# Kernel optimization log

Hardware: AMD Instinct MI355X
Metric: run time of the kernel (lower is better)

Reference implementation:

```python
import jax, jax.numpy as jnp
import numpy as np

HIDDEN = 768
FFN = 3072
E = 8
TOP_K = 2


def setup_inputs() -> dict:
    key = jax.random.key(0)
    k_x, k_r, k_w1, k_w2 = jax.random.split(key, 4)
    x = jax.random.normal(k_x, (1, 1024, HIDDEN), dtype=jnp.float32)
    # nn.Linear(hidden, E, bias=False): weight applied as x @ W^T; store as [H, E]
    bound = 1.0 / np.sqrt(HIDDEN)
    router_w = jax.random.uniform(k_r, (HIDDEN, E), minval=-bound, maxval=bound, dtype=jnp.float32)
    w1 = jax.random.normal(k_w1, (E, HIDDEN, FFN), dtype=jnp.float32) * 0.02
    w2 = jax.random.normal(k_w2, (E, FFN, HIDDEN), dtype=jnp.float32) * 0.02
    return {"x": x, "router_w": router_w, "w1": w1, "w2": w2}


def reference(x, router_w, w1, w2):
    B, T, H = x.shape
    xf = x.reshape(-1, H)                                  # [N, H]
    logits = xf @ router_w                                 # [N, E] (eval mode: no noise)
    probs = jax.nn.softmax(logits, axis=-1)
    top_v, top_i = jax.lax.top_k(probs, TOP_K)             # [N, K]
    top_v = top_v / jnp.sum(top_v, axis=-1, keepdims=True)  # renormalize top-k probs
    # Combine top-k weights into a dense per-expert gate; zero gates make the
    # dense per-expert computation mathematically identical to sparse dispatch.
    gates = jnp.sum(jax.nn.one_hot(top_i, E, dtype=xf.dtype) * top_v[..., None], axis=1)  # [N, E]
    h = jax.nn.gelu(jnp.einsum('nh,ehf->enf', xf, w1), approximate=False)  # [E, N, F]
    y = jnp.einsum('enf,efh->enh', h, w2)                  # [E, N, H]
    out = jnp.einsum('ne,enh->nh', gates, y)               # [N, H]
    return out.reshape(B, T, H)
```

## Files before the change

kernel.cpp:

```cpp
#include <hip/hip_runtime.h>
#include <cmath>

#define NTOK 1024
#define HD   768
#define FF   3072
#define NE   8
#define NSLOT (NTOK * 2)

typedef unsigned short u16;
typedef unsigned int   u32;
typedef __bf16 bf16x8 __attribute__((ext_vector_type(8)));
typedef float  f32x4  __attribute__((ext_vector_type(4)));

__device__ __forceinline__ u16 f2bf(float f) {
  union { float f; u32 u; } v; v.f = f;
  u32 r = v.u + 0x7FFFu + ((v.u >> 16) & 1u);
  return (u16)(r >> 16);
}

__global__ __launch_bounds__(256) void router_logits(
    const float* __restrict__ x, const float* __restrict__ rw,
    u16* __restrict__ xb, int* __restrict__ counts,
    int* __restrict__ ti, int* __restrict__ tpos, float* __restrict__ tg)
{
  __shared__ float rwt[NE * HD];
  const int tid = threadIdx.x;
  for (int i = tid; i < NE * HD; i += 256) {
    const int h = i >> 3, e = i & 7;
    rwt[e * HD + h] = rw[i];
  }
  __syncthreads();

  const int wid  = tid >> 6;
  const int lane = tid & 63;
  const int t    = blockIdx.x * 4 + wid;
  const float* xrow = x + (size_t)t * HD;
  u16* xbrow = xb + (size_t)t * HD;

  float acc[NE] = {};
#pragma unroll
  for (int j = 0; j < 12; ++j) {
    const int h = lane + j * 64;
    const float xv = xrow[h];
    xbrow[h] = f2bf(xv);
#pragma unroll
    for (int e = 0; e < NE; ++e) acc[e] += xv * rwt[e * HD + h];
  }
#pragma unroll
  for (int e = 0; e < NE; ++e) {
    float v = acc[e];
#pragma unroll
    for (int off = 32; off; off >>= 1) v += __shfl_down(v, off, 64);
    acc[e] = v;
  }

  if (lane == 0) {
    float v0 = -1e30f, v1 = -1e30f; int i0 = 0, i1 = 0;
#pragma unroll
    for (int e = 0; e < NE; ++e) {
      const float p = acc[e];
      if (p > v0) { v1 = v0; i1 = i0; v0 = p; i0 = e; }
      else if (p > v1) { v1 = p; i1 = e; }
    }
    const float e1 = expf(v1 - v0);
    const float g0 = 1.0f / (1.0f + e1);
    const float g1 = e1 / (1.0f + e1);
    const int p0 = atomicAdd(&counts[i0], 1);
    const int p1 = atomicAdd(&counts[i1], 1);
    ti[2 * t] = i0;  ti[2 * t + 1] = i1;
    tpos[2 * t] = p0; tpos[2 * t + 1] = p1;
    tg[2 * t] = g0;  tg[2 * t + 1] = g1;
  }
}

__global__ __launch_bounds__(1024) void router_scatter(
    const int* __restrict__ counts, const int* __restrict__ ti,
    const int* __restrict__ tpos, const float* __restrict__ tg,
    int* __restrict__ tos, float* __restrict__ gos, int* __restrict__ seg)
{
  __shared__ int offs[NE];
  const int t = threadIdx.x;
  if (t == 0) {
    int o = 0;
    for (int e = 0; e < NE; ++e) {
      offs[e] = o; seg[e] = o; seg[NE + e] = counts[e]; o += counts[e];
    }
  }
  __syncthreads();
  const int i0 = ti[2 * t], i1 = ti[2 * t + 1];
  const int s0 = offs[i0] + tpos[2 * t];
  const int s1 = offs[i1] + tpos[2 * t + 1];
  tos[s0] = t; gos[s0] = tg[2 * t];
  tos[s1] = t; gos[s1] = tg[2 * t + 1];
}

#define LDA 40

__global__ __launch_bounds__(256) void ffn1_kernel(
    const u16* __restrict__ xb, const float* __restrict__ w1,
    const int* __restrict__ tos, const int* __restrict__ seg,
    u16* __restrict__ hbuf)
{
  const int e   = blockIdx.z;
  const int cnt = seg[NE + e];
  const int m0  = blockIdx.y * 64;
  if (m0 >= cnt) return;
  const int start = seg[e];
  const int n0    = blockIdx.x * 64;

  __shared__ __align__(16) u16 As[64 * LDA];
  __shared__ __align__(16) u16 Bs[64 * LDA];
  __shared__ int toks[64];

  const int tid = threadIdx.x;
  if (tid < 64) toks[tid] = tos[start + min(m0 + tid, cnt - 1)];
  __syncthreads();

  const int lane = tid & 63;
  const int wid  = tid >> 6;
  const int wm   = (wid >> 1) << 5;
  const int wn   = (wid & 1) << 5;
  const int q    = lane >> 4;
  const int r16  = lane & 15;

  const int am = tid >> 2;
  const int ak = (tid & 3) << 3;
  const u16* arow = xb + (size_t)toks[am] * HD + ak;
  const int bkw = wid << 3;

  f32x4 acc[2][2] = {};

  for (int k0 = 0; k0 < HD; k0 += 32) {
    {
      const uint4 av = *(const uint4*)(arow + k0);
      *(uint4*)(&As[am * LDA + ak]) = av;
    }
    {
      const float* src = w1 + (size_t)(e * HD + k0 + bkw) * FF + n0 + lane;
      u16 tmp[8];
#pragma unroll
      for (int j = 0; j < 8; ++j) tmp[j] = f2bf(src[(size_t)j * FF]);
      uint4 bv;
      bv.x = (u32)tmp[0] | ((u32)tmp[1] << 16);
      bv.y = (u32)tmp[2] | ((u32)tmp[3] << 16);
      bv.z = (u32)tmp[4] | ((u32)tmp[5] << 16);
      bv.w = (u32)tmp[6] | ((u32)tmp[7] << 16);
      *(uint4*)(&Bs[lane * LDA + bkw]) = bv;
    }
    __syncthreads();
    bf16x8 af0 = *(const bf16x8*)(&As[(wm + r16)      * LDA + (q << 3)]);
    bf16x8 af1 = *(const bf16x8*)(&As[(wm + 16 + r16) * LDA + (q << 3)]);
    bf16x8 bf0 = *(const bf16x8*)(&Bs[(wn + r16)      * LDA + (q << 3)]);
    bf16x8 bf1 = *(const bf16x8*)(&Bs[(wn + 16 + r16) * LDA + (q << 3)]);
    acc[0][0] = __builtin_amdgcn_mfma_f32_16x16x32_bf16(af0, bf0, acc[0][0], 0, 0, 0);
    acc[0][1] = __builtin_amdgcn_mfma_f32_16x16x32_bf16(af0, bf1, acc[0][1], 0, 0, 0);
    acc[1][0] = __builtin_amdgcn_mfma_f32_16x16x32_bf16(af1, bf0, acc[1][0], 0, 0, 0);
    acc[1][1] = __builtin_amdgcn_mfma_f32_16x16x32_bf16(af1, bf1, acc[1][1], 0, 0, 0);
    __syncthreads();
  }

#pragma unroll
  for (int r = 0; r < 2; ++r) {
#pragma unroll
    for (int i = 0; i < 4; ++i) {
      const int mloc = wm + r * 16 + q * 4 + i;
      if (m0 + mloc < cnt) {
        u16* drow = hbuf + (size_t)(start + m0 + mloc) * FF + n0;
#pragma unroll
        for (int c = 0; c < 2; ++c) {
          float v = acc[r][c][i];
          v = 0.5f * v * (1.0f + erff(v * 0.70710678118f));
          drow[wn + c * 16 + r16] = f2bf(v);
        }
      }
    }
  }
}

__global__ __launch_bounds__(256) void ffn2_kernel(
    const u16* __restrict__ hbuf, const float* __restrict__ w2,
    const int* __restrict__ tos, const float* __restrict__ gos,
    const int* __restrict__ seg, float* __restrict__ out)
{
  const int e   = blockIdx.z;
  const int cnt = seg[NE + e];
  const int m0  = blockIdx.y * 64;
  if (m0 >= cnt) return;
  const int start = seg[e];
  const int n0    = blockIdx.x * 64;

  __shared__ __align__(16) u16 As[64 * LDA];
  __shared__ __align__(16) u16 Bs[64 * LDA];
  __shared__ int   toks[64];
  __shared__ float gates[64];

  const int tid = threadIdx.x;
  if (tid < 64) {
    const int idx = start + min(m0 + tid, cnt - 1);
    toks[tid]  = tos[idx];
    gates[tid] = gos[idx];
  }

  const int lane = tid & 63;
  const int wid  = tid >> 6;
  const int wm   = (wid >> 1) << 5;
  const int wn   = (wid & 1) << 5;
  const int q    = lane >> 4;
  const int r16  = lane & 15;

  const int am = tid >> 2;
  const int ak = (tid & 3) << 3;
  const u16* arow = hbuf + (size_t)(start + min(m0 + am, cnt - 1)) * FF + ak;
  const int bkw = wid << 3;

  f32x4 acc[2][2] = {};

  for (int k0 = 0; k0 < FF; k0 += 32) {
    {
      const uint4 av = *(const uint4*)(arow + k0);
      *(uint4*)(&As[am * LDA + ak]) = av;
    }
    {
      const float* src = w2 + (size_t)(e * FF + k0 + bkw) * HD + n0 + lane;
      u16 tmp[8];
#pragma unroll
      for (int j = 0; j < 8; ++j) tmp[j] = f2bf(src[(size_t)j * HD]);
      uint4 bv;
      bv.x = (u32)tmp[0] | ((u32)tmp[1] << 16);
      bv.y = (u32)tmp[2] | ((u32)tmp[3] << 16);
      bv.z = (u32)tmp[4] | ((u32)tmp[5] << 16);
      bv.w = (u32)tmp[6] | ((u32)tmp[7] << 16);
      *(uint4*)(&Bs[lane * LDA + bkw]) = bv;
    }
    __syncthreads();
    bf16x8 af0 = *(const bf16x8*)(&As[(wm + r16)      * LDA + (q << 3)]);
    bf16x8 af1 = *(const bf16x8*)(&As[(wm + 16 + r16) * LDA + (q << 3)]);
    bf16x8 bf0 = *(const bf16x8*)(&Bs[(wn + r16)      * LDA + (q << 3)]);
    bf16x8 bf1 = *(const bf16x8*)(&Bs[(wn + 16 + r16) * LDA + (q << 3)]);
    acc[0][0] = __builtin_amdgcn_mfma_f32_16x16x32_bf16(af0, bf0, acc[0][0], 0, 0, 0);
    acc[0][1] = __builtin_amdgcn_mfma_f32_16x16x32_bf16(af0, bf1, acc[0][1], 0, 0, 0);
    acc[1][0] = __builtin_amdgcn_mfma_f32_16x16x32_bf16(af1, bf0, acc[1][0], 0, 0, 0);
    acc[1][1] = __builtin_amdgcn_mfma_f32_16x16x32_bf16(af1, bf1, acc[1][1], 0, 0, 0);
    __syncthreads();
  }

#pragma unroll
  for (int r = 0; r < 2; ++r) {
#pragma unroll
    for (int i = 0; i < 4; ++i) {
      const int mloc = wm + r * 16 + q * 4 + i;
      if (m0 + mloc < cnt) {
        const int tok  = toks[mloc];
        const float g  = gates[mloc];
        float* drow = out + (size_t)tok * HD + n0;
#pragma unroll
        for (int c = 0; c < 2; ++c) {
          atomicAdd(drow + wn + c * 16 + r16, g * acc[r][c][i]);
        }
      }
    }
  }
}

extern "C" void kernel_launch(void* const* d_in, const int* in_sizes, int n_in,
                              void* d_out, int out_size, void* d_ws, size_t ws_size,
                              hipStream_t stream) {
  const float* x  = (const float*)d_in[0];
  const float* rw = (const float*)d_in[1];
  const float* w1 = (const float*)d_in[2];
  const float* w2 = (const float*)d_in[3];
  float* out = (float*)d_out;

  char* ws = (char*)d_ws;
  const size_t o_xb    = 0;
  const size_t o_hbuf  = o_xb + (size_t)NTOK * HD * 2;
  const size_t o_tos   = o_hbuf + (size_t)NSLOT * FF * 2;
  const size_t o_gos   = o_tos + (size_t)NSLOT * 4;
  const size_t o_seg   = o_gos + (size_t)NSLOT * 4;
  const size_t o_cnt   = o_seg + 64 * 4;
  const size_t o_ti    = o_cnt + NE * 4;
  const size_t o_tpos  = o_ti + (size_t)NSLOT * 4;
  const size_t o_tg    = o_tpos + (size_t)NSLOT * 4;
  u16*   xb    = (u16*)(ws + o_xb);
  u16*   hbuf  = (u16*)(ws + o_hbuf);
  int*   tos   = (int*)(ws + o_tos);
  float* gos   = (float*)(ws + o_gos);
  int*   seg   = (int*)(ws + o_seg);
  int*   cnts  = (int*)(ws + o_cnt);
  int*   ti    = (int*)(ws + o_ti);
  int*   tpos  = (int*)(ws + o_tpos);
  float* tg    = (float*)(ws + o_tg);

  hipMemsetAsync(d_out, 0, (size_t)NTOK * HD * sizeof(float), stream);
  hipMemsetAsync(cnts, 0, NE * sizeof(int), stream);
  hipLaunchKernelGGL(router_logits, dim3(NTOK / 4), dim3(256), 0, stream,
                     x, rw, xb, cnts, ti, tpos, tg);
  hipLaunchKernelGGL(router_scatter, dim3(1), dim3(1024), 0, stream,
                     cnts, ti, tpos, tg, tos, gos, seg);
  hipLaunchKernelGGL(ffn1_kernel, dim3(FF / 64, NTOK / 64, NE), dim3(256), 0, stream,
                     xb, w1, tos, seg, hbuf);
  hipLaunchKernelGGL(ffn2_kernel, dim3(HD / 64, NTOK / 64, NE), dim3(256), 0, stream,
                     hbuf, w2, tos, gos, seg, out);
}
```

Measured before the change: 318.6 us.

## Register-prefetch next K tile, widen BK to 64, split-K ffn2

Both FFN GEMM kernels now load the next K-slice of activations and fp32 weights into registers while MFMAs run on the current shared-memory tile, so global latency overlaps compute. The K tile grows from 32 to 64, which halves the number of barrier pairs per output. ffn2 is split along K into two halves across the grid z dimension, doubling its block count for occupancy; the existing atomicAdd epilogue merges the partial sums. The costs are more registers per thread and twice as many atomic adds into the output.

After: 270.7 us. 15.0% less time.

```diff
diff --git a/kernel.cpp b/kernel.cpp
--- a/kernel.cpp
+++ b/kernel.cpp
@@ -6,6 +6,8 @@
 #define FF   3072
 #define NE   8
 #define NSLOT (NTOK * 2)
+#define BK   64
+#define LDK  72
 
 typedef unsigned short u16;
 typedef unsigned int   u32;
@@ -16,6 +18,15 @@
   union { float f; u32 u; } v; v.f = f;
   u32 r = v.u + 0x7FFFu + ((v.u >> 16) & 1u);
   return (u16)(r >> 16);
+}
+
+__device__ __forceinline__ uint4 pack8(const float* b) {
+  uint4 r;
+  r.x = (u32)f2bf(b[0]) | ((u32)f2bf(b[1]) << 16);
+  r.y = (u32)f2bf(b[2]) | ((u32)f2bf(b[3]) << 16);
+  r.z = (u32)f2bf(b[4]) | ((u32)f2bf(b[5]) << 16);
+  r.w = (u32)f2bf(b[6]) | ((u32)f2bf(b[7]) << 16);
+  return r;
 }
 
 __global__ __launch_bounds__(256) void router_logits(
@@ -94,8 +105,6 @@
   tos[s1] = t; gos[s1] = tg[2 * t + 1];
 }
 
-#define LDA 40
-
 __global__ __launch_bounds__(256) void ffn1_kernel(
     const u16* __restrict__ xb, const float* __restrict__ w1,
     const int* __restrict__ tos, const int* __restrict__ seg,
@@ -108,13 +117,26 @@
   const int start = seg[e];
   const int n0    = blockIdx.x * 64;
 
-  __shared__ __align__(16) u16 As[64 * LDA];
-  __shared__ __align__(16) u16 Bs[64 * LDA];
+  __shared__ __align__(16) u16 As[64 * LDK];
+  __shared__ __align__(16) u16 Bs[64 * LDK];
   __shared__ int toks[64];
 
   const int tid = threadIdx.x;
   if (tid < 64) toks[tid] = tos[start + min(m0 + tid, cnt - 1)];
   __syncthreads();
+
+  const int ar  = tid >> 3;
+  const int akc = (tid & 7) << 3;
+  const u16* asrc0 = xb + (size_t)toks[ar]      * HD + akc;
+  const u16* asrc1 = xb + (size_t)toks[ar + 32] * HD + akc;
+  const int adst0 = ar * LDK + akc;
+  const int adst1 = (ar + 32) * LDK + akc;
+  const int bn  = tid & 63;
+  const int bkc = (tid >> 6) << 3;
+  const float* bsrc0 = w1 + ((size_t)e * HD + bkc) * FF + n0 + bn;
+  const float* bsrc1 = bsrc0 + (size_t)32 * FF;
+  const int bdst0 = bn * LDK + bkc;
+  const int bdst1 = bn * LDK + bkc + 32;
 
   const int lane = tid & 63;
   const int wid  = tid >> 6;
@@ -123,40 +145,46 @@
   const int q    = lane >> 4;
   const int r16  = lane & 15;
 
-  const int am = tid >> 2;
-  const int ak = (tid & 3) << 3;
-  const u16* arow = xb + (size_t)toks[am] * HD + ak;
-  const int bkw = wid << 3;
-
+  uint4 areg0, areg1;
+  float breg0[8], breg1[8];
+
+#define FFN_LOAD(K0)                                                        \
+  do {                                                                      \
+    areg0 = *(const uint4*)(asrc0 + (K0));                                  \
+    areg1 = *(const uint4*)(asrc1 + (K0));                                  \
+    _Pragma("unroll")                                                       \
+    for (int j = 0; j < 8; ++j) breg0[j] = bsrc0[(size_t)((K0) + j) * FF];  \
+    _Pragma("unroll")                                                       \
+    for (int j = 0; j < 8; ++j) breg1[j] = bsrc1[(size_t)((K0) + j) * FF];  \
+  } while (0)
+
+  FFN_LOAD(0);
   f32x4 acc[2][2] = {};
 
-  for (int k0 = 0; k0 < HD; k0 += 32) {
-    {
-      const uint4 av = *(const uint4*)(arow + k0);
-      *(uint4*)(&As[am * LDA + ak]) = av;
-    }
-    {
-      const float* src = w1 + (size_t)(e * HD + k0 + bkw) * FF + n0 + lane;
-      u16 tmp[8];
-#pragma unroll
-      for (int j = 0; j < 8; ++j) tmp[j] = f2bf(src[(size_t)j * FF]);
-      uint4 bv;
-      bv.x = (u32)tmp[0] | ((u32)tmp[1] << 16);
-      bv.y = (u32)tmp[2] | ((u32)tmp[3] << 16);
-      bv.z = (u32)tmp[4] | ((u32)tmp[5] << 16);
-      bv.w = (u32)tmp[6] | ((u32)tmp[7] << 16);
-      *(uint4*)(&Bs[lane * LDA + bkw]) = bv;
-    }
+  for (int k0 = 0;;) {
+    const uint4 bw0 = pack8(breg0);
+    const uint4 bw1 = pack8(breg1);
     __syncthreads();
-    bf16x8 af0 = *(const bf16x8*)(&As[(wm + r16)      * LDA + (q << 3)]);
-    bf16x8 af1 = *(const bf16x8*)(&As[(wm + 16 + r16) * LDA + (q << 3)]);
-    bf16x8 bf0 = *(const bf16x8*)(&Bs[(wn + r16)      * LDA + (q << 3)]);
-    bf16x8 bf1 = *(const bf16x8*)(&Bs[(wn + 16 + r16) * LDA + (q << 3)]);
-    acc[0][0] = __builtin_amdgcn_mfma_f32_16x16x32_bf16(af0, bf0, acc[0][0], 0, 0, 0);
-    acc[0][1] = __builtin_amdgcn_mfma_f32_16x16x32_bf16(af0, bf1, acc[0][1], 0, 0, 0);
-    acc[1][0] = __builtin_amdgcn_mfma_f32_16x16x32_bf16(af1, bf0, acc[1][0], 0, 0, 0);
-    acc[1][1] = __builtin_amdgcn_mfma_f32_16x16x32_bf16(af1, bf1, acc[1][1], 0, 0, 0);
+    *(uint4*)(&As[adst0]) = areg0;
+    *(uint4*)(&As[adst1]) = areg1;
+    *(uint4*)(&Bs[bdst0]) = bw0;
+    *(uint4*)(&Bs[bdst1]) = bw1;
     __syncthreads();
+    k0 += BK;
+    if (k0 < HD) { FFN_LOAD(k0); }
+#pragma unroll
+    for (int s = 0; s < 2; ++s) {
+      const int ko = s * 32 + (q << 3);
+      bf16x8 a0 = *(const bf16x8*)(&As[(wm + r16)      * LDK + ko]);
+      bf16x8 a1 = *(const bf16x8*)(&As[(wm + 16 + r16) * LDK + ko]);
+      bf16x8 b0 = *(const bf16x8*)(&Bs[(wn + r16)      * LDK + ko]);
+      bf16x8 b1 = *(const bf16x8*)(&Bs[(wn + 16 + r16) * LDK + ko]);
+      acc[0][0] = __builtin_amdgcn_mfma_f32_16x16x32_bf16(a0, b0, acc[0][0], 0, 0, 0);
+      acc[0][1] = __builtin_amdgcn_mfma_f32_16x16x32_bf16(a0, b1, acc[0][1], 0, 0, 0);
+      acc[1][0] = __builtin_amdgcn_mfma_f32_16x16x32_bf16(a1, b0, acc[1][0], 0, 0, 0);
+      acc[1][1] = __builtin_amdgcn_mfma_f32_16x16x32_bf16(a1, b1, acc[1][1], 0, 0, 0);
+    }
+    if (k0 >= HD) break;
   }
 
 #pragma unroll
@@ -177,20 +205,26 @@
   }
 }
 
+#define KSPLIT 2
+#define KSEG   (FF / KSPLIT)
+
 __global__ __launch_bounds__(256) void ffn2_kernel(
     const u16* __restrict__ hbuf, const float* __restrict__ w2,
     const int* __restrict__ tos, const float* __restrict__ gos,
     const int* __restrict__ seg, float* __restrict__ out)
 {
-  const int e   = blockIdx.z;
+  const int ez  = blockIdx.z;
+  const int e   = ez >> 1;
+  const int ks  = ez & 1;
   const int cnt = seg[NE + e];
   const int m0  = blockIdx.y * 64;
   if (m0 >= cnt) return;
   const int start = seg[e];
   const int n0    = blockIdx.x * 64;
-
-  __shared__ __align__(16) u16 As[64 * LDA];
-  __shared__ __align__(16) u16 Bs[64 * LDA];
+  const int kbase = ks * KSEG;
+
+  __shared__ __align__(16) u16 As[64 * LDK];
+  __shared__ __align__(16) u16 Bs[64 * LDK];
   __shared__ int   toks[64];
   __shared__ float gates[64];
 
@@ -200,6 +234,20 @@
     toks[tid]  = tos[idx];
     gates[tid] = gos[idx];
   }
+  __syncthreads();
+
+  const int ar  = tid >> 3;
+  const int akc = (tid & 7) << 3;
+  const u16* asrc0 = hbuf + (size_t)(start + min(m0 + ar,      cnt - 1)) * FF + kbase + akc;
+  const u16* asrc1 = hbuf + (size_t)(start + min(m0 + ar + 32, cnt - 1)) * FF + kbase + akc;
+  const int adst0 = ar * LDK + akc;
+  const int adst1 = (ar + 32) * LDK + akc;
+  const int bn  = tid & 63;
+  const int bkc = (tid >> 6) << 3;
+  const float* bsrc0 = w2 + ((size_t)e * FF + kbase + bkc) * HD + n0 + bn;
+  const float* bsrc1 = bsrc0 + (size_t)32 * HD;
+  const int bdst0 = bn * LDK + bkc;
+  const int bdst1 = bn * LDK + bkc + 32;
 
   const int lane = tid & 63;
   const int wid  = tid >> 6;
@@ -208,40 +256,46 @@
   const int q    = lane >> 4;
   const int r16  = lane & 15;
 
-  const int am = tid >> 2;
-  const int ak = (tid & 3) << 3;
-  const u16* arow = hbuf + (size_t)(start + min(m0 + am, cnt - 1)) * FF + ak;
-  const int bkw = wid << 3;
-
+  uint4 areg0, areg1;
+  float breg0[8], breg1[8];
+
+#define FFN2_LOAD(K0)                                                       \
+  do {                                                                      \
+    areg0 = *(const uint4*)(asrc0 + (K0));                                  \
+    areg1 = *(const uint4*)(asrc1 + (K0));                                  \
+    _Pragma("unroll")                                                       \
+    for (int j = 0; j < 8; ++j) breg0[j] = bsrc0[(size_t)((K0) + j) * HD];  \
+    _Pragma("unroll")                                                       \
+    for (int j = 0; j < 8; ++j) breg1[j] = bsrc1[(size_t)((K0) + j) * HD];  \
+  } while (0)
+
+  FFN2_LOAD(0);
   f32x4 acc[2][2] = {};
 
-  for (int k0 = 0; k0 < FF; k0 += 32) {
-    {
-      const uint4 av = *(const uint4*)(arow + k0);
-      *(uint4*)(&As[am * LDA + ak]) = av;
-    }
-    {
-      const float* src = w2 + (size_t)(e * FF + k0 + bkw) * HD + n0 + lane;
-      u16 tmp[8];
-#pragma unroll
-      for (int j = 0; j < 8; ++j) tmp[j] = f2bf(src[(size_t)j * HD]);
-      uint4 bv;
-      bv.x = (u32)tmp[0] | ((u32)tmp[1] << 16);
-      bv.y = (u32)tmp[2] | ((u32)tmp[3] << 16);
-      bv.z = (u32)tmp[4] | ((u32)tmp[5] << 16);
-      bv.w = (u32)tmp[6] | ((u32)tmp[7] << 16);
-      *(uint4*)(&Bs[lane * LDA + bkw]) = bv;
-    }
+  for (int k0 = 0;;) {
+    const uint4 bw0 = pack8(breg0);
+    const uint4 bw1 = pack8(breg1);
     __syncthreads();
-    bf16x8 af0 = *(const bf16x8*)(&As[(wm + r16)      * LDA + (q << 3)]);
-    bf16x8 af1 = *(const bf16x8*)(&As[(wm + 16 + r16) * LDA + (q << 3)]);
-    bf16x8 bf0 = *(const bf16x8*)(&Bs[(wn + r16)      * LDA + (q << 3)]);
-    bf16x8 bf1 = *(const bf16x8*)(&Bs[(wn + 16 + r16) * LDA + (q << 3)]);
-    acc[0][0] = __builtin_amdgcn_mfma_f32_16x16x32_bf16(af0, bf0, acc[0][0], 0, 0, 0);
-    acc[0][1] = __builtin_amdgcn_mfma_f32_16x16x32_bf16(af0, bf1, acc[0][1], 0, 0, 0);
-    acc[1][0] = __builtin_amdgcn_mfma_f32_16x16x32_bf16(af1, bf0, acc[1][0], 0, 0, 0);
-    acc[1][1] = __builtin_amdgcn_mfma_f32_16x16x32_bf16(af1, bf1, acc[1][1], 0, 0, 0);
+    *(uint4*)(&As[adst0]) = areg0;
+    *(uint4*)(&As[adst1]) = areg1;
+    *(uint4*)(&Bs[bdst0]) = bw0;
+    *(uint4*)(&Bs[bdst1]) = bw1;
     __syncthreads();
+    k0 += BK;
+    if (k0 < KSEG) { FFN2_LOAD(k0); }
+#pragma unroll
+    for (int s = 0; s < 2; ++s) {
+      const int ko = s * 32 + (q << 3);
+      bf16x8 a0 = *(const bf16x8*)(&As[(wm + r16)      * LDK + ko]);
+      bf16x8 a1 = *(const bf16x8*)(&As[(wm + 16 + r16) * LDK + ko]);
+      bf16x8 b0 = *(const bf16x8*)(&Bs[(wn + r16)      * LDK + ko]);
+      bf16x8 b1 = *(const bf16x8*)(&Bs[(wn + 16 + r16) * LDK + ko]);
+      acc[0][0] = __builtin_amdgcn_mfma_f32_16x16x32_bf16(a0, b0, acc[0][0], 0, 0, 0);
+      acc[0][1] = __builtin_amdgcn_mfma_f32_16x16x32_bf16(a0, b1, acc[0][1], 0, 0, 0);
+      acc[1][0] = __builtin_amdgcn_mfma_f32_16x16x32_bf16(a1, b0, acc[1][0], 0, 0, 0);
+      acc[1][1] = __builtin_amdgcn_mfma_f32_16x16x32_bf16(a1, b1, acc[1][1], 0, 0, 0);
+    }
+    if (k0 >= KSEG) break;
   }
 
 #pragma unroll
@@ -299,6 +353,6 @@
                      cnts, ti, tpos, tg, tos, gos, seg);
   hipLaunchKernelGGL(ffn1_kernel, dim3(FF / 64, NTOK / 64, NE), dim3(256), 0, stream,
                      xb, w1, tos, seg, hbuf);
-  hipLaunchKernelGGL(ffn2_kernel, dim3(HD / 64, NTOK / 64, NE), dim3(256), 0, stream,
+  hipLaunchKernelGGL(ffn2_kernel, dim3(HD / 64, NTOK / 64, NE * KSPLIT), dim3(256), 0, stream,
                      hbuf, w2, tos, gos, seg, out);
 }
```

## Pre-convert weights to transposed bf16, use direct-to-LDS loads, split-K FFN2

Applied to the files above, without the earlier changes.

Adds a pre-pass kernel that converts the fp32 w1/w2 weights to bf16 and transposes them to K-contiguous order in workspace. The GEMM kernels can then stream tiles into shared memory with global_load_lds 16-byte loads into an XOR-swizzled 64-wide K tile, instead of doing strided fp32 loads and converting per block. FFN2 is also split two ways along K to raise the block count, relying on its existing atomic accumulation. The pre-pass adds an extra read and write of all weights every call, and the split adds more atomics.

After: 279.6 us. 1.14x faster.

```diff
diff --git a/kernel.cpp b/kernel.cpp
--- a/kernel.cpp
+++ b/kernel.cpp
@@ -6,6 +6,7 @@
 #define FF   3072
 #define NE   8
 #define NSLOT (NTOK * 2)
+#define BK   64
 
 typedef unsigned short u16;
 typedef unsigned int   u32;
@@ -16,6 +17,41 @@
   union { float f; u32 u; } v; v.f = f;
   u32 r = v.u + 0x7FFFu + ((v.u >> 16) & 1u);
   return (u16)(r >> 16);
+}
+
+__device__ __forceinline__ void load16(const void* g, void* l) {
+  __builtin_amdgcn_global_load_lds(
+      (const __attribute__((address_space(1))) u32*)g,
+      (__attribute__((address_space(3))) u32*)l, 16, 0, 0);
+}
+
+__global__ __launch_bounds__(256) void convert_t_kernel(
+    const float* __restrict__ src, u16* __restrict__ dst, int K, int N)
+{
+  const int e  = blockIdx.z;
+  const int n0 = blockIdx.x * 64;
+  const int k0 = blockIdx.y * 64;
+  __shared__ u16 lt[64][65];
+  const int tid = threadIdx.x;
+  const int rr = tid >> 4;
+  const int cc = (tid & 15) << 2;
+  const float* s = src + (size_t)e * K * N;
+#pragma unroll
+  for (int j = 0; j < 4; ++j) {
+    const int k = j * 16 + rr;
+    const float4 v = *(const float4*)(s + (size_t)(k0 + k) * N + n0 + cc);
+    lt[cc + 0][k] = f2bf(v.x); lt[cc + 1][k] = f2bf(v.y);
+    lt[cc + 2][k] = f2bf(v.z); lt[cc + 3][k] = f2bf(v.w);
+  }
+  __syncthreads();
+  u16* d = dst + (size_t)e * N * K;
+#pragma unroll
+  for (int j = 0; j < 4; ++j) {
+    const int n = j * 16 + rr;
+    ushort4 o;
+    o.x = lt[n][cc]; o.y = lt[n][cc + 1]; o.z = lt[n][cc + 2]; o.w = lt[n][cc + 3];
+    *(ushort4*)(d + (size_t)(n0 + n) * K + k0 + cc) = o;
+  }
 }
 
 __global__ __launch_bounds__(256) void router_logits(
@@ -94,10 +130,9 @@
   tos[s1] = t; gos[s1] = tg[2 * t + 1];
 }
 
-#define LDA 40
 
 __global__ __launch_bounds__(256) void ffn1_kernel(
-    const u16* __restrict__ xb, const float* __restrict__ w1,
+    const u16* __restrict__ xb, const u16* __restrict__ w1t,
     const int* __restrict__ tos, const int* __restrict__ seg,
     u16* __restrict__ hbuf)
 {
@@ -108,8 +143,8 @@
   const int start = seg[e];
   const int n0    = blockIdx.x * 64;
 
-  __shared__ __align__(16) u16 As[64 * LDA];
-  __shared__ __align__(16) u16 Bs[64 * LDA];
+  __shared__ __align__(16) u16 As[64 * 64];
+  __shared__ __align__(16) u16 Bs[64 * 64];
   __shared__ int toks[64];
 
   const int tid = threadIdx.x;
@@ -118,44 +153,44 @@
 
   const int lane = tid & 63;
   const int wid  = tid >> 6;
-  const int wm   = (wid >> 1) << 5;
-  const int wn   = (wid & 1) << 5;
-  const int q    = lane >> 4;
-  const int r16  = lane & 15;
-
-  const int am = tid >> 2;
-  const int ak = (tid & 3) << 3;
-  const u16* arow = xb + (size_t)toks[am] * HD + ak;
-  const int bkw = wid << 3;
+
+  const int r0 = wid * 8 + (lane >> 3);
+  const int p  = lane & 7;
+  const int c  = p ^ (r0 & 7);
+  const u16* ag0 = xb + (size_t)toks[r0]      * HD + c * 8;
+  const u16* ag1 = xb + (size_t)toks[r0 + 32] * HD + c * 8;
+  const u16* bg0 = w1t + ((size_t)e * FF + n0 + r0)      * HD + c * 8;
+  const u16* bg1 = w1t + ((size_t)e * FF + n0 + r0 + 32) * HD + c * 8;
+  u16* al0 = As + (wid * 8) * 64;
+  u16* al1 = As + (wid * 8 + 32) * 64;
+  u16* bl0 = Bs + (wid * 8) * 64;
+  u16* bl1 = Bs + (wid * 8 + 32) * 64;
+
+  const int wm  = (wid >> 1) << 5;
+  const int wn  = (wid & 1) << 5;
+  const int q   = lane >> 4;
+  const int r16 = lane & 15;
 
   f32x4 acc[2][2] = {};
 
-  for (int k0 = 0; k0 < HD; k0 += 32) {
-    {
-      const uint4 av = *(const uint4*)(arow + k0);
-      *(uint4*)(&As[am * LDA + ak]) = av;
-    }
-    {
-      const float* src = w1 + (size_t)(e * HD + k0 + bkw) * FF + n0 + lane;
-      u16 tmp[8];
-#pragma unroll
-      for (int j = 0; j < 8; ++j) tmp[j] = f2bf(src[(size_t)j * FF]);
-      uint4 bv;
-      bv.x = (u32)tmp[0] | ((u32)tmp[1] << 16);
-      bv.y = (u32)tmp[2] | ((u32)tmp[3] << 16);
-      bv.z = (u32)tmp[4] | ((u32)tmp[5] << 16);
-      bv.w = (u32)tmp[6] | ((u32)tmp[7] << 16);
-      *(uint4*)(&Bs[lane * LDA + bkw]) = bv;
-    }
+  for (int k0 = 0; k0 < HD; k0 += BK) {
+    load16(ag0 + k0, al0);
+    load16(ag1 + k0, al1);
+    load16(bg0 + k0, bl0);
+    load16(bg1 + k0, bl1);
     __syncthreads();
-    bf16x8 af0 = *(const bf16x8*)(&As[(wm + r16)      * LDA + (q << 3)]);
-    bf16x8 af1 = *(const bf16x8*)(&As[(wm + 16 + r16) * LDA + (q << 3)]);
-    bf16x8 bf0 = *(const bf16x8*)(&Bs[(wn + r16)      * LDA + (q << 3)]);
-    bf16x8 bf1 = *(const bf16x8*)(&Bs[(wn + 16 + r16) * LDA + (q << 3)]);
-    acc[0][0] = __builtin_amdgcn_mfma_f32_16x16x32_bf16(af0, bf0, acc[0][0], 0, 0, 0);
-    acc[0][1] = __builtin_amdgcn_mfma_f32_16x16x32_bf16(af0, bf1, acc[0][1], 0, 0, 0);
-    acc[1][0] = __builtin_amdgcn_mfma_f32_16x16x32_bf16(af1, bf0, acc[1][0], 0, 0, 0);
-    acc[1][1] = __builtin_amdgcn_mfma_f32_16x16x32_bf16(af1, bf1, acc[1][1], 0, 0, 0);
+#pragma unroll
+    for (int s = 0; s < 2; ++s) {
+      const int pa = ((s << 2) + q) ^ (r16 & 7);
+      bf16x8 a0 = *(const bf16x8*)(&As[(wm + r16)      * 64 + (pa << 3)]);
+      bf16x8 a1 = *(const bf16x8*)(&As[(wm + 16 + r16) * 64 + (pa << 3)]);
+      bf16x8 b0 = *(const bf16x8*)(&Bs[(wn + r16)      * 64 + (pa << 3)]);
+      bf16x8 b1 = *(const bf16x8*)(&Bs[(wn + 16 + r16) * 64 + (pa << 3)]);
+      acc[0][0] = __builtin_amdgcn_mfma_f32_16x16x32_bf16(a0, b0, acc[0][0], 0, 0, 0);
+      acc[0][1] = __builtin_amdgcn_mfma_f32_16x16x32_bf16(a0, b1, acc[0][1], 0, 0, 0);
+      acc[1][0] = __builtin_amdgcn_mfma_f32_16x16x32_bf16(a1, b0, acc[1][0], 0, 0, 0);
+      acc[1][1] = __builtin_amdgcn_mfma_f32_16x16x32_bf16(a1, b1, acc[1][1], 0, 0, 0);
+    }
     __syncthreads();
   }
 
@@ -167,30 +202,36 @@
       if (m0 + mloc < cnt) {
         u16* drow = hbuf + (size_t)(start + m0 + mloc) * FF + n0;
 #pragma unroll
-        for (int c = 0; c < 2; ++c) {
-          float v = acc[r][c][i];
+        for (int cix = 0; cix < 2; ++cix) {
+          float v = acc[r][cix][i];
           v = 0.5f * v * (1.0f + erff(v * 0.70710678118f));
-          drow[wn + c * 16 + r16] = f2bf(v);
+          drow[wn + cix * 16 + r16] = f2bf(v);
         }
       }
     }
   }
 }
 
+#define KSPLIT 2
+#define KSEG   (FF / KSPLIT)
+
 __global__ __launch_bounds__(256) void ffn2_kernel(
-    const u16* __restrict__ hbuf, const float* __restrict__ w2,
+    const u16* __restrict__ hbuf, const u16* __restrict__ w2t,
     const int* __restrict__ tos, const float* __restrict__ gos,
     const int* __restrict__ seg, float* __restrict__ out)
 {
-  const int e   = blockIdx.z;
+  const int ez  = blockIdx.z;
+  const int e   = ez >> 1;
+  const int ks  = ez & 1;
   const int cnt = seg[NE + e];
   const int m0  = blockIdx.y * 64;
   if (m0 >= cnt) return;
   const int start = seg[e];
   const int n0    = blockIdx.x * 64;
-
-  __shared__ __align__(16) u16 As[64 * LDA];
-  __shared__ __align__(16) u16 Bs[64 * LDA];
+  const int kbase = ks * KSEG;
+
+  __shared__ __align__(16) u16 As[64 * 64];
+  __shared__ __align__(16) u16 Bs[64 * 64];
   __shared__ int   toks[64];
   __shared__ float gates[64];
 
@@ -200,47 +241,48 @@
     toks[tid]  = tos[idx];
     gates[tid] = gos[idx];
   }
+  __syncthreads();
 
   const int lane = tid & 63;
   const int wid  = tid >> 6;
-  const int wm   = (wid >> 1) << 5;
-  const int wn   = (wid & 1) << 5;
-  const int q    = lane >> 4;
-  const int r16  = lane & 15;
-
-  const int am = tid >> 2;
-  const int ak = (tid & 3) << 3;
-  const u16* arow = hbuf + (size_t)(start + min(m0 + am, cnt - 1)) * FF + ak;
-  const int bkw = wid << 3;
+
+  const int r0 = wid * 8 + (lane >> 3);
+  const int p  = lane & 7;
+  const int c  = p ^ (r0 & 7);
+  const u16* ag0 = hbuf + (size_t)(start + min(m0 + r0,      cnt - 1)) * FF + kbase + c * 8;
+  const u16* ag1 = hbuf + (size_t)(start + min(m0 + r0 + 32, cnt - 1)) * FF + kbase + c * 8;
+  const u16* bg0 = w2t + ((size_t)e * HD + n0 + r0)      * FF + kbase + c * 8;
+  const u16* bg1 = w2t + ((size_t)e * HD + n0 + r0 + 32) * FF + kbase + c * 8;
+  u16* al0 = As + (wid * 8) * 64;
+  u16* al1 = As + (wid * 8 + 32) * 64;
+  u16* bl0 = Bs + (wid * 8) * 64;
+  u16* bl1 = Bs + (wid * 8 + 32) * 64;
+
+  const int wm  = (wid >> 1) << 5;
+  const int wn  = (wid & 1) << 5;
+  const int q   = lane >> 4;
+  const int r16 = lane & 15;
 
   f32x4 acc[2][2] = {};
 
-  for (int k0 = 0; k0 < FF; k0 += 32) {
-    {
-      const uint4 av = *(const uint4*)(arow + k0);
-      *(uint4*)(&As[am * LDA + ak]) = av;
-    }
-    {
-      const float* src = w2 + (size_t)(e * FF + k0 + bkw) * HD + n0 + lane;
-      u16 tmp[8];
-#pragma unroll
-      for (int j = 0; j < 8; ++j) tmp[j] = f2bf(src[(size_t)j * HD]);
-      uint4 bv;
-      bv.x = (u32)tmp[0] | ((u32)tmp[1] << 16);
-      bv.y = (u32)tmp[2] | ((u32)tmp[3] << 16);
-      bv.z = (u32)tmp[4] | ((u32)tmp[5] << 16);
-      bv.w = (u32)tmp[6] | ((u32)tmp[7] << 16);
-      *(uint4*)(&Bs[lane * LDA + bkw]) = bv;
-    }
+  for (int k0 = 0; k0 < KSEG; k0 += BK) {
+    load16(ag0 + k0, al0);
+    load16(ag1 + k0, al1);
+    load16(bg0 + k0, bl0);
+    load16(bg1 + k0, bl1);
     __syncthreads();
-    bf16x8 af0 = *(const bf16x8*)(&As[(wm + r16)      * LDA + (q << 3)]);
-    bf16x8 af1 = *(const bf16x8*)(&As[(wm + 16 + r16) * LDA + (q << 3)]);
-    bf16x8 bf0 = *(const bf16x8*)(&Bs[(wn + r16)      * LDA + (q << 3)]);
-    bf16x8 bf1 = *(const bf16x8*)(&Bs[(wn + 16 + r16) * LDA + (q << 3)]);
-    acc[0][0] = __builtin_amdgcn_mfma_f32_16x16x32_bf16(af0, bf0, acc[0][0], 0, 0, 0);
-    acc[0][1] = __builtin_amdgcn_mfma_f32_16x16x32_bf16(af0, bf1, acc[0][1], 0, 0, 0);
-    acc[1][0] = __builtin_amdgcn_mfma_f32_16x16x32_bf16(af1, bf0, acc[1][0], 0, 0, 0);
-    acc[1][1] = __builtin_amdgcn_mfma_f32_16x16x32_bf16(af1, bf1, acc[1][1], 0, 0, 0);
+#pragma unroll
+    for (int s = 0; s < 2; ++s) {
+      const int pa = ((s << 2) + q) ^ (r16 & 7);
+      bf16x8 a0 = *(const bf16x8*)(&As[(wm + r16)      * 64 + (pa << 3)]);
+      bf16x8 a1 = *(const bf16x8*)(&As[(wm + 16 + r16) * 64 + (pa << 3)]);
+      bf16x8 b0 = *(const bf16x8*)(&Bs[(wn + r16)      * 64 + (pa << 3)]);
+      bf16x8 b1 = *(const bf16x8*)(&Bs[(wn + 16 + r16) * 64 + (pa << 3)]);
+      acc[0][0] = __builtin_amdgcn_mfma_f32_16x16x32_bf16(a0, b0, acc[0][0], 0, 0, 0);
+      acc[0][1] = __builtin_amdgcn_mfma_f32_16x16x32_bf16(a0, b1, acc[0][1], 0, 0, 0);
+      acc[1][0] = __builtin_amdgcn_mfma_f32_16x16x32_bf16(a1, b0, acc[1][0], 0, 0, 0);
+      acc[1][1] = __builtin_amdgcn_mfma_f32_16x16x32_bf16(a1, b1, acc[1][1], 0, 0, 0);
+    }
     __syncthreads();
   }
 
@@ -254,8 +296,8 @@
         const float g  = gates[mloc];
         float* drow = out + (size_t)tok * HD + n0;
 #pragma unroll
-        for (int c = 0; c < 2; ++c) {
-          atomicAdd(drow + wn + c * 16 + r16, g * acc[r][c][i]);
+        for (int cix = 0; cix < 2; ++cix) {
+          atomicAdd(drow + wn + cix * 16 + r16, g * acc[r][cix][i]);
         }
       }
     }
@@ -281,6 +323,8 @@
   const size_t o_ti    = o_cnt + NE * 4;
   const size_t o_tpos  = o_ti + (size_t)NSLOT * 4;
   const size_t o_tg    = o_tpos + (size_t)NSLOT * 4;
+  const size_t o_w1t   = (o_tg + (size_t)NSLOT * 4 + 255) & ~(size_t)255;
+  const size_t o_w2t   = o_w1t + (size_t)NE * HD * FF * 2;
   u16*   xb    = (u16*)(ws + o_xb);
   u16*   hbuf  = (u16*)(ws + o_hbuf);
   int*   tos   = (int*)(ws + o_tos);
@@ -290,15 +334,21 @@
   int*   ti    = (int*)(ws + o_ti);
   int*   tpos  = (int*)(ws + o_tpos);
   float* tg    = (float*)(ws + o_tg);
+  u16*   w1t   = (u16*)(ws + o_w1t);
+  u16*   w2t   = (u16*)(ws + o_w2t);
 
   hipMemsetAsync(d_out, 0, (size_t)NTOK * HD * sizeof(float), stream);
   hipMemsetAsync(cnts, 0, NE * sizeof(int), stream);
+  hipLaunchKernelGGL(convert_t_kernel, dim3(FF / 64, HD / 64, NE), dim3(256), 0, stream,
+                     w1, w1t, HD, FF);
+  hipLaunchKernelGGL(convert_t_kernel, dim3(HD / 64, FF / 64, NE), dim3(256), 0, stream,
+                     w2, w2t, FF, HD);
   hipLaunchKernelGGL(router_logits, dim3(NTOK / 4), dim3(256), 0, stream,
                      x, rw, xb, cnts, ti, tpos, tg);
   hipLaunchKernelGGL(router_scatter, dim3(1), dim3(1024), 0, stream,
                      cnts, ti, tpos, tg, tos, gos, seg);
   hipLaunchKernelGGL(ffn1_kernel, dim3(FF / 64, NTOK / 64, NE), dim3(256), 0, stream,
-                     xb, w1, tos, seg, hbuf);
-  hipLaunchKernelGGL(ffn2_kernel, dim3(HD / 64, NTOK / 64, NE), dim3(256), 0, stream,
-                     hbuf, w2, tos, gos, seg, out);
-}
+                     xb, w1t, tos, seg, hbuf);
+  hipLaunchKernelGGL(ffn2_kernel, dim3(HD / 64, NTOK / 64, NE * KSPLIT), dim3(256), 0, stream,
+                     hbuf, w2t, tos, gos, seg, out);
+}
```
